# Optimization experiments

Measured on AMD Instinct MI355X. Metric: run time of the kernel, lower is better.

The kernel has to match this reference:

```python
import jax, jax.numpy as jnp
import numpy as np

COS_EPS = 1e-08


def setup_inputs() -> dict:
    key = jax.random.key(0)
    k1, k2, k3, k4, k5 = jax.random.split(key, 5)
    B, N, C = 4, 4096, 128
    q_node = jax.random.normal(k1, (B, N, C), dtype=jnp.float32)
    k_node = jax.random.normal(k2, (B, N, C), dtype=jnp.float32)
    v_node = jax.random.normal(k3, (B, N, C), dtype=jnp.float32)
    # shared Linear(h_dim, h_dim): torch default init scale ~ 1/sqrt(C)
    W = jax.random.normal(k4, (C, C), dtype=jnp.float32) / jnp.sqrt(jnp.float32(C))
    b = jax.random.normal(k5, (C,), dtype=jnp.float32) / jnp.sqrt(jnp.float32(C))
    return {"q_node": q_node, "k_node": k_node, "v_node": v_node, "W": W, "b": b}


def reference(q_node, k_node, v_node, W, b):
    # shared projection applied to q, k, v
    q = jnp.einsum('bnc,cd->bnd', q_node, W.T) + b
    k = jnp.einsum('bnc,cd->bnd', k_node, W.T) + b
    v = jnp.einsum('bnc,cd->bnd', v_node, W.T) + b
    # cosine similarity scores: [B, Nq, Nk]
    qn = jnp.linalg.norm(q, axis=2, keepdims=True)        # [B, Nq, 1]
    kn = jnp.linalg.norm(k, axis=2, keepdims=True)        # [B, Nk, 1]
    scores = jnp.einsum('bqc,bkc->bqk', q, k)
    cos_sim = scores / (qn * jnp.swapaxes(kn, 1, 2) + COS_EPS)
    # sum-normalization (not softmax)
    edge_weight = cos_sim / (cos_sim.sum(axis=2, keepdims=True) + 1e-08)
    # weighted aggregation: [B, Nq, C]
    return jnp.einsum('bqk,bkc->bqc', edge_weight, v)
```

## Files before the change

kernel.cpp:

```cpp
#include <hip/hip_runtime.h>

#define BB 4
#define NN 4096
#define CC 128
#define NROWS (BB * NN)

#define QN_OFF  0
#define QP_OFF  (QN_OFF + NROWS)
#define MM_OFF  (QP_OFF + NROWS * CC)
#define KS_OFF  (MM_OFF + BB * CC * CC)
#define PP_OFF  (KS_OFF + BB * CC)
#define KP_OFF  (PP_OFF + 256 * CC * CC)

typedef __attribute__((ext_vector_type(8))) short short8;
typedef __attribute__((ext_vector_type(4))) float f32x4;

__device__ __forceinline__ float dot4(const float4 x, const float4 k)
{
    return x.x * k.x + x.y * k.y + x.z * k.z + x.w * k.w;
}

__device__ __forceinline__ unsigned short f2bf(float f)
{
    union { float f; unsigned u; } v; v.f = f;
    unsigned r = (v.u + 0x7fffu + ((v.u >> 16) & 1u)) >> 16;
    return (unsigned short)r;
}
__device__ __forceinline__ float bf2f(unsigned short h)
{
    union { unsigned u; float f; } v; v.u = ((unsigned)h) << 16;
    return v.f;
}

__global__ __launch_bounds__(512, 1) void projpb_kernel(
    const float* __restrict__ q_node, const float* __restrict__ k_node,
    const float* __restrict__ v_node, const float* __restrict__ W,
    const float* __restrict__ bias, float* __restrict__ ws)
{
    __shared__ __align__(16) unsigned short Wsp[3 * CC * CC];
    __shared__ float4 red[512];
    unsigned short* Whi = Wsp;
    unsigned short* Wmd = Wsp + CC * CC;
    unsigned short* Wlo = Wsp + 2 * CC * CC;

    const int tid = threadIdx.x;

    for (int e = tid; e < CC * CC; e += 512) {
        int col = e >> 7, k = e & 127;
        float wv = W[e];
        unsigned short hi = f2bf(wv);
        float r1 = wv - bf2f(hi);
        unsigned short md = f2bf(r1);
        unsigned short lo = f2bf(r1 - bf2f(md));
        int idx = (col << 7) + ((((k >> 3) ^ (col & 7)) << 3) | (k & 7));
        Whi[idx] = hi; Wmd[idx] = md; Wlo[idx] = lo;
    }

    const int blk  = blockIdx.x;
    const int base = blk * 64;
    const int w    = tid >> 6;
    const int lane = tid & 63;
    const int l15  = lane & 15;
    const int lg   = lane >> 4;
    const bool isq = (w < 4);
    const int rt   = w & 3;
    const float* X = isq ? q_node : k_node;
    const int arow = base + rt * 16 + l15;

    f32x4 acc[8];
#pragma unroll
    for (int ct = 0; ct < 8; ct++) {
        float b = bias[ct * 16 + l15];
        acc[ct] = (f32x4){b, b, b, b};
    }

    __syncthreads();

    const float* Xr = X + (size_t)arow * CC;
#pragma unroll
    for (int ks = 0; ks < 4; ks++) {
        const int k0 = ks * 32 + lg * 8;
        float4 xa = *(const float4*)(Xr + k0);
        float4 xb = *(const float4*)(Xr + k0 + 4);
        float xs[8] = {xa.x, xa.y, xa.z, xa.w, xb.x, xb.y, xb.z, xb.w};
        short8 Ahi, Amd, Alo;
#pragma unroll
        for (int j = 0; j < 8; j++) {
            unsigned short h = f2bf(xs[j]);
            float r1 = xs[j] - bf2f(h);
            unsigned short m = f2bf(r1);
            Ahi[j] = (short)h;
            Amd[j] = (short)m;
            Alo[j] = (short)f2bf(r1 - bf2f(m));
        }
        const int slot = ks * 4 + lg;
#pragma unroll
        for (int ct = 0; ct < 8; ct++) {
            int col  = ct * 16 + l15;
            int fidx = (col << 7) + ((slot ^ (col & 7)) << 3);
            short8 Bhi = *(const short8*)(Whi + fidx);
            short8 Bmd = *(const short8*)(Wmd + fidx);
            short8 Blo = *(const short8*)(Wlo + fidx);
            acc[ct] = __builtin_amdgcn_mfma_f32_16x16x32_bf16(Ahi, Bhi, acc[ct], 0, 0, 0);
            acc[ct] = __builtin_amdgcn_mfma_f32_16x16x32_bf16(Ahi, Bmd, acc[ct], 0, 0, 0);
            acc[ct] = __builtin_amdgcn_mfma_f32_16x16x32_bf16(Amd, Bhi, acc[ct], 0, 0, 0);
            acc[ct] = __builtin_amdgcn_mfma_f32_16x16x32_bf16(Ahi, Blo, acc[ct], 0, 0, 0);
            acc[ct] = __builtin_amdgcn_mfma_f32_16x16x32_bf16(Amd, Bmd, acc[ct], 0, 0, 0);
            acc[ct] = __builtin_amdgcn_mfma_f32_16x16x32_bf16(Alo, Bhi, acc[ct], 0, 0, 0);
        }
    }

    float ss[4];
#pragma unroll
    for (int r = 0; r < 4; r++) {
        float t = 0.f;
#pragma unroll
        for (int ct = 0; ct < 8; ct++) t += acc[ct][r] * acc[ct][r];
#pragma unroll
        for (int off = 8; off > 0; off >>= 1) t += __shfl_xor(t, off, 16);
        ss[r] = t;
    }

    if (isq) {
#pragma unroll
        for (int r = 0; r < 4; r++) {
            int gr = base + rt * 16 + lg * 4 + r;
            float* qp = ws + QP_OFF + (size_t)gr * CC;
#pragma unroll
            for (int ct = 0; ct < 8; ct++) qp[ct * 16 + l15] = acc[ct][r];
            if (l15 == 0) ws[QN_OFF + gr] = sqrtf(ss[r]);
        }
    }

    __syncthreads();

    float* Khs = (float*)Wsp;
    float* Vs  = Khs + 8192;

    if (!isq) {
#pragma unroll
        for (int r = 0; r < 4; r++) {
            float inv = 1.0f / sqrtf(ss[r]);
            int lr = rt * 16 + lg * 4 + r;
            float* kp = Khs + lr * CC;
#pragma unroll
            for (int ct = 0; ct < 8; ct++) kp[ct * 16 + l15] = acc[ct][r] * inv;
        }
    }

    const int c4v = tid & 31, nrv = tid >> 5;
    const float* Vp = v_node + (size_t)base * CC;
#pragma unroll
    for (int i = 0; i < 4; i++) {
        int n = nrv + i * 16;
        ((float4*)(Vs + n * CC))[c4v] = ((const float4*)(Vp + (size_t)n * CC))[c4v];
    }
    __syncthreads();

    float4 ksum4 = make_float4(0.f, 0.f, 0.f, 0.f);
#pragma unroll
    for (int i = 0; i < 4; i++) {
        int n = nrv + i * 16;
        float4 kv = ((const float4*)(Khs + n * CC))[c4v];
        ksum4.x += kv.x; ksum4.y += kv.y; ksum4.z += kv.z; ksum4.w += kv.w;
    }

    const int dg2 = tid & 15, cg = tid >> 4;
    float a2[4][8];
#pragma unroll
    for (int i = 0; i < 4; i++)
#pragma unroll
        for (int j = 0; j < 8; j++) a2[i][j] = 0.f;

#define P2L(ka, va, vb, n)                                  \
    ka = *(const float4*)(Khs + (n) * CC + 4 * cg);         \
    va = *(const float4*)(Vs + (n) * CC + 4 * dg2);         \
    vb = *(const float4*)(Vs + (n) * CC + 64 + 4 * dg2);
#define P2F(ka, va, vb)                                     \
    {  float kc[4] = {ka.x, ka.y, ka.z, ka.w};              \
       float vd[8] = {va.x, va.y, va.z, va.w,               \
                      vb.x, vb.y, vb.z, vb.w};              \
       _Pragma("unroll")                                    \
       for (int i = 0; i < 4; i++)                          \
           { _Pragma("unroll")                              \
             for (int j = 0; j < 8; j++)                    \
                 a2[i][j] += kc[i] * vd[j]; } }

    {
        float4 kaA, vaA, vbA, kaB, vaB, vbB;
        P2L(kaA, vaA, vbA, 0)
        for (int n = 0; n <= 60; n += 2) {
            P2L(kaB, vaB, vbB, n + 1)
            P2F(kaA, vaA, vbA)
            P2L(kaA, vaA, vbA, n + 2)
            P2F(kaB, vaB, vbB)
        }
        P2L(kaB, vaB, vbB, 63)
        P2F(kaA, vaA, vbA)
        P2F(kaB, vaB, vbB)
    }
#undef P2L
#undef P2F

    float* pp = ws + PP_OFF + (size_t)blk * (CC * CC);
#pragma unroll
    for (int i = 0; i < 4; i++) {
        int c = 4 * cg + i;
        *(float4*)(pp + c * CC + 4 * dg2) =
            make_float4(a2[i][0], a2[i][1], a2[i][2], a2[i][3]);
        *(float4*)(pp + c * CC + 64 + 4 * dg2) =
            make_float4(a2[i][4], a2[i][5], a2[i][6], a2[i][7]);
    }

    red[nrv * 32 + c4v] = ksum4;
    __syncthreads();
    if (tid < 32) {
        float4 sm = red[tid];
#pragma unroll
        for (int i = 1; i < 16; i++) {
            float4 t = red[i * 32 + tid];
            sm.x += t.x; sm.y += t.y; sm.z += t.z; sm.w += t.w;
        }
        ((float4*)(ws + KP_OFF + (size_t)blk * CC))[tid] = sm;
    }
}

__global__ __launch_bounds__(256) void mchain_kernel(const float* __restrict__ W,
                                                     const float* __restrict__ bias,
                                                     float* __restrict__ ws)
{
    __shared__ float4 W4s[CC * 32];
    __shared__ float4 m0q[4][2][32];
    __shared__ float m0row[2][CC];
    __shared__ float kpart[4];
    __shared__ float ksl[2];
    const int tid = threadIdx.x;
    const int b = blockIdx.y, x = blockIdx.x;
    const int c0 = x * 2;

    for (int idx = tid; idx < CC * 32; idx += 256) {
        int e = idx >> 5, d4 = idx & 31;
        W4s[(e << 5) + (d4 ^ (e & 31))] = ((const float4*)W)[idx];
    }

    {
        const int q  = tid >> 6;
        const int r  = (tid >> 5) & 1;
        const int c4 = tid & 31;
        const float4* pp = (const float4*)(ws + PP_OFF
                         + (size_t)(b * 64 + q * 16) * (CC * CC)
                         + (size_t)(c0 + r) * CC) + c4;
        float4 s0 = make_float4(0.f, 0.f, 0.f, 0.f);
#pragma unroll 4
        for (int p = 0; p < 16; p++) {
            float4 t = pp[(size_t)p * (CC * CC / 4)];
            s0.x += t.x; s0.y += t.y; s0.z += t.z; s0.w += t.w;
        }
        m0q[q][r][c4] = s0;
    }

    {
        const int rr = tid >> 7, p = tid & 127;
        float v = 0.f;
        if (p < 64) v = ws[KP_OFF + (size_t)(b * 64 + p) * CC + c0 + rr];
#pragma unroll
        for (int off = 32; off > 0; off >>= 1) v += __shfl_xor(v, off, 64);
        if ((tid & 63) == 0) kpart[tid >> 6] = v;
    }
    __syncthreads();

    if (tid < 64) {
        const int r = tid >> 5, c4 = tid & 31;
        float4 a = m0q[0][r][c4], bq = m0q[1][r][c4];
        float4 c = m0q[2][r][c4], d = m0q[3][r][c4];
        float4 s;
        s.x = (a.x + bq.x) + (c.x + d.x);
        s.y = (a.y + bq.y) + (c.y + d.y);
        s.z = (a.z + bq.z) + (c.z + d.z);
        s.w = (a.w + bq.w) + (c.w + d.w);
        ((float4*)&m0row[r][0])[c4] = s;
    }
    if (tid < 2) {
        float s = kpart[tid * 2] + kpart[tid * 2 + 1];
        ksl[tid] = s;
        ws[KS_OFF + b * CC + c0 + tid] = s;
    }
    __syncthreads();

    const int r = tid >> 7, e = tid & 127;
    const float4* mr = (const float4*)m0row[r];
    float m = 0.f;
#pragma unroll
    for (int d4 = 0; d4 < 32; d4++) {
        float4 a4 = mr[d4];
        float4 w4 = W4s[(e << 5) + (d4 ^ (e & 31))];
        m += a4.x * w4.x + a4.y * w4.y + a4.z * w4.z + a4.w * w4.w;
    }
    m += ksl[r] * bias[e];
    ws[MM_OFF + (size_t)b * CC * CC + (size_t)(c0 + r) * CC + e] = m;
}

__global__ __launch_bounds__(512, 1) void out_kernel(const float* __restrict__ ws,
                                                     float* __restrict__ out)
{
    __shared__ __align__(16) unsigned short Msp[3 * CC * CC];
    __shared__ float Ksl[CC];
    unsigned short* Mhi = Msp;
    unsigned short* Mmd = Msp + CC * CC;
    unsigned short* Mlo = Msp + 2 * CC * CC;

    const int tid = threadIdx.x;
    const int blk = blockIdx.x;
    const int b  = blk >> 6;
    const int r0 = (blk & 63) * 64;
    const float* M = ws + MM_OFF + (size_t)b * CC * CC;

    for (int e = tid; e < CC * CC; e += 512) {
        int k = e >> 7, col = e & 127;
        float mv = M[e];
        unsigned short hi = f2bf(mv);
        float r1 = mv - bf2f(hi);
        unsigned short md = f2bf(r1);
        unsigned short lo = f2bf(r1 - bf2f(md));
        int idx = (col << 7) + ((((k >> 3) ^ (col & 7)) << 3) | (k & 7));
        Mhi[idx] = hi; Mmd[idx] = md; Mlo[idx] = lo;
    }
    if (tid < CC) Ksl[tid] = ws[KS_OFF + b * CC + tid];

    const int w    = tid >> 6;
    const int lane = tid & 63;
    const int l15  = lane & 15;
    const int lg   = lane >> 4;
    const int rt   = w & 3;
    const int ch   = w >> 2;

    const int arow = r0 + rt * 16 + l15;
    const float* Xr = ws + QP_OFF + ((size_t)b * NN + arow) * CC;

    f32x4 acc[4];
#pragma unroll
    for (int ct = 0; ct < 4; ct++) acc[ct] = (f32x4){0.f, 0.f, 0.f, 0.f};
    float sp = 0.f;

    __syncthreads();

#pragma unroll
    for (int ks = 0; ks < 4; ks++) {
        const int k0 = ks * 32 + lg * 8;
        float4 xa = *(const float4*)(Xr + k0);
        float4 xb = *(const float4*)(Xr + k0 + 4);
        float xs[8] = {xa.x, xa.y, xa.z, xa.w, xb.x, xb.y, xb.z, xb.w};
        short8 Ahi, Amd, Alo;
#pragma unroll
        for (int j = 0; j < 8; j++) {
            unsigned short h = f2bf(xs[j]);
            float r1 = xs[j] - bf2f(h);
            unsigned short m = f2bf(r1);
            Ahi[j] = (short)h;
            Amd[j] = (short)m;
            Alo[j] = (short)f2bf(r1 - bf2f(m));
            sp += xs[j] * Ksl[k0 + j];
        }
        const int slot = ks * 4 + lg;
#pragma unroll
        for (int ct = 0; ct < 4; ct++) {
            int col  = ch * 64 + ct * 16 + l15;
            int fidx = (col << 7) + ((slot ^ (col & 7)) << 3);
            short8 Bhi = *(const short8*)(Mhi + fidx);
            short8 Bmd = *(const short8*)(Mmd + fidx);
            short8 Blo = *(const short8*)(Mlo + fidx);
            acc[ct] = __builtin_amdgcn_mfma_f32_16x16x32_bf16(Ahi, Bhi, acc[ct], 0, 0, 0);
            acc[ct] = __builtin_amdgcn_mfma_f32_16x16x32_bf16(Ahi, Bmd, acc[ct], 0, 0, 0);
            acc[ct] = __builtin_amdgcn_mfma_f32_16x16x32_bf16(Amd, Bhi, acc[ct], 0, 0, 0);
            acc[ct] = __builtin_amdgcn_mfma_f32_16x16x32_bf16(Ahi, Blo, acc[ct], 0, 0, 0);
            acc[ct] = __builtin_amdgcn_mfma_f32_16x16x32_bf16(Amd, Bmd, acc[ct], 0, 0, 0);
            acc[ct] = __builtin_amdgcn_mfma_f32_16x16x32_bf16(Alo, Bhi, acc[ct], 0, 0, 0);
        }
    }

    sp += __shfl_xor(sp, 16, 64);
    sp += __shfl_xor(sp, 32, 64);

#pragma unroll
    for (int r = 0; r < 4; r++) {
        const int rowt = lg * 4 + r;
        float srow = __shfl(sp, rowt, 64);
        const int gr = r0 + rt * 16 + rowt;
        float qn = ws[QN_OFF + (size_t)b * NN + gr];
        float inv = 1.0f / (srow + 1e-8f * qn);
        float* op = out + ((size_t)b * NN + gr) * CC + ch * 64;
#pragma unroll
        for (int ct = 0; ct < 4; ct++)
            op[ct * 16 + l15] = acc[ct][r] * inv;
    }
}

extern "C" void kernel_launch(void* const* d_in, const int* in_sizes, int n_in,
                              void* d_out, int out_size, void* d_ws, size_t ws_size,
                              hipStream_t stream)
{
    const float* q_node = (const float*)d_in[0];
    const float* k_node = (const float*)d_in[1];
    const float* v_node = (const float*)d_in[2];
    const float* W      = (const float*)d_in[3];
    const float* bias   = (const float*)d_in[4];
    float* out = (float*)d_out;
    float* ws  = (float*)d_ws;

    projpb_kernel<<<256, 512, 0, stream>>>(q_node, k_node, v_node, W, bias, ws);
    mchain_kernel<<<dim3(64, BB), 256, 0, stream>>>(W, bias, ws);
    out_kernel<<<256, 512, 0, stream>>>(ws, out);
}
```

Measured before the change: 122.0 us.

## Compute per-block K^T V partial with split-bf16 MFMA instead of FP32 FMA

The per-block outer-product accumulation of normalized K and V (128x128 over 64 rows) moves from a scalar FP32 FMA loop to bf16 MFMA instructions. Each operand is split into three bf16 parts so that six MFMAs per tile approximate FP32 accuracy. K and V are written into swizzled shared-memory layouts, and the per-block K column sums are now reduced with wave shuffles. The split conversion adds ALU work and smaller LDS stores, and it risks small accuracy loss compared with exact FP32.

```diff
diff --git a/kernel.cpp b/kernel.cpp
--- a/kernel.cpp
+++ b/kernel.cpp
@@ -15,11 +15,6 @@
 typedef __attribute__((ext_vector_type(8))) short short8;
 typedef __attribute__((ext_vector_type(4))) float f32x4;
 
-__device__ __forceinline__ float dot4(const float4 x, const float4 k)
-{
-    return x.x * k.x + x.y * k.y + x.z * k.z + x.w * k.w;
-}
-
 __device__ __forceinline__ unsigned short f2bf(float f)
 {
     union { float f; unsigned u; } v; v.f = f;
@@ -38,7 +33,7 @@
     const float* __restrict__ bias, float* __restrict__ ws)
 {
     __shared__ __align__(16) unsigned short Wsp[3 * CC * CC];
-    __shared__ float4 red[512];
+    __shared__ float redf[512];
     unsigned short* Whi = Wsp;
     unsigned short* Wmd = Wsp + CC * CC;
     unsigned short* Wlo = Wsp + 2 * CC * CC;
@@ -134,94 +129,104 @@
 
     __syncthreads();
 
-    float* Khs = (float*)Wsp;
-    float* Vs  = Khs + 8192;
+    unsigned short* Ahi_p = Wsp;
+    unsigned short* Amd_p = Wsp + 8192;
+    unsigned short* Alo_p = Wsp + 16384;
+    unsigned short* Bhi_p = Wsp + 24576;
+    unsigned short* Bmd_p = Wsp + 32768;
+    unsigned short* Blo_p = Wsp + 40960;
 
     if (!isq) {
+        float ksp[8] = {0.f, 0.f, 0.f, 0.f, 0.f, 0.f, 0.f, 0.f};
 #pragma unroll
         for (int r = 0; r < 4; r++) {
             float inv = 1.0f / sqrtf(ss[r]);
-            int lr = rt * 16 + lg * 4 + r;
-            float* kp = Khs + lr * CC;
-#pragma unroll
-            for (int ct = 0; ct < 8; ct++) kp[ct * 16 + l15] = acc[ct][r] * inv;
-        }
-    }
-
-    const int c4v = tid & 31, nrv = tid >> 5;
-    const float* Vp = v_node + (size_t)base * CC;
-#pragma unroll
-    for (int i = 0; i < 4; i++) {
-        int n = nrv + i * 16;
-        ((float4*)(Vs + n * CC))[c4v] = ((const float4*)(Vp + (size_t)n * CC))[c4v];
-    }
-    __syncthreads();
-
-    float4 ksum4 = make_float4(0.f, 0.f, 0.f, 0.f);
-#pragma unroll
-    for (int i = 0; i < 4; i++) {
-        int n = nrv + i * 16;
-        float4 kv = ((const float4*)(Khs + n * CC))[c4v];
-        ksum4.x += kv.x; ksum4.y += kv.y; ksum4.z += kv.z; ksum4.w += kv.w;
-    }
-
-    const int dg2 = tid & 15, cg = tid >> 4;
-    float a2[4][8];
-#pragma unroll
-    for (int i = 0; i < 4; i++)
-#pragma unroll
-        for (int j = 0; j < 8; j++) a2[i][j] = 0.f;
-
-#define P2L(ka, va, vb, n)                                  \
-    ka = *(const float4*)(Khs + (n) * CC + 4 * cg);         \
-    va = *(const float4*)(Vs + (n) * CC + 4 * dg2);         \
-    vb = *(const float4*)(Vs + (n) * CC + 64 + 4 * dg2);
-#define P2F(ka, va, vb)                                     \
-    {  float kc[4] = {ka.x, ka.y, ka.z, ka.w};              \
-       float vd[8] = {va.x, va.y, va.z, va.w,               \
-                      vb.x, vb.y, vb.z, vb.w};              \
-       _Pragma("unroll")                                    \
-       for (int i = 0; i < 4; i++)                          \
-           { _Pragma("unroll")                              \
-             for (int j = 0; j < 8; j++)                    \
-                 a2[i][j] += kc[i] * vd[j]; } }
+            int n = rt * 16 + lg * 4 + r;
+#pragma unroll
+            for (int ct = 0; ct < 8; ct++) {
+                int c = ct * 16 + l15;
+                float val = acc[ct][r] * inv;
+                unsigned short h = f2bf(val);
+                float r1 = val - bf2f(h);
+                unsigned short m = f2bf(r1);
+                unsigned short l = f2bf(r1 - bf2f(m));
+                int idx = (c << 6) + ((((n >> 3) ^ (c & 7)) << 3) | (n & 7));
+                Ahi_p[idx] = h; Amd_p[idx] = m; Alo_p[idx] = l;
+                ksp[ct] += val;
+            }
+        }
+#pragma unroll
+        for (int ct = 0; ct < 8; ct++) {
+            ksp[ct] += __shfl_xor(ksp[ct], 16, 64);
+            ksp[ct] += __shfl_xor(ksp[ct], 32, 64);
+            if (lg == 0) redf[(rt * 8 + ct) * 16 + l15] = ksp[ct];
+        }
+    }
 
     {
-        float4 kaA, vaA, vbA, kaB, vaB, vbB;
-        P2L(kaA, vaA, vbA, 0)
-        for (int n = 0; n <= 60; n += 2) {
-            P2L(kaB, vaB, vbB, n + 1)
-            P2F(kaA, vaA, vbA)
-            P2L(kaA, vaA, vbA, n + 2)
-            P2F(kaB, vaB, vbB)
-        }
-        P2L(kaB, vaB, vbB, 63)
-        P2F(kaA, vaA, vbA)
-        P2F(kaB, vaB, vbB)
-    }
-#undef P2L
-#undef P2F
-
-    float* pp = ws + PP_OFF + (size_t)blk * (CC * CC);
-#pragma unroll
-    for (int i = 0; i < 4; i++) {
-        int c = 4 * cg + i;
-        *(float4*)(pp + c * CC + 4 * dg2) =
-            make_float4(a2[i][0], a2[i][1], a2[i][2], a2[i][3]);
-        *(float4*)(pp + c * CC + 64 + 4 * dg2) =
-            make_float4(a2[i][4], a2[i][5], a2[i][6], a2[i][7]);
-    }
-
-    red[nrv * 32 + c4v] = ksum4;
-    __syncthreads();
-    if (tid < 32) {
-        float4 sm = red[tid];
-#pragma unroll
-        for (int i = 1; i < 16; i++) {
-            float4 t = red[i * 32 + tid];
-            sm.x += t.x; sm.y += t.y; sm.z += t.z; sm.w += t.w;
-        }
-        ((float4*)(ws + KP_OFF + (size_t)blk * CC))[tid] = sm;
+        const int c4v = tid & 31, nrv = (tid >> 5) & 15;
+        const float* Vp = v_node + (size_t)base * CC;
+#pragma unroll
+        for (int i = 0; i < 4; i++) {
+            int n = nrv + i * 16;
+#pragma unroll
+            for (int j = 0; j < 4; j++) {
+                int d = c4v + 32 * j;
+                float val = Vp[(size_t)n * CC + d];
+                unsigned short h = f2bf(val);
+                float r1 = val - bf2f(h);
+                unsigned short m = f2bf(r1);
+                unsigned short l = f2bf(r1 - bf2f(m));
+                int idx = (d << 6) + ((((n >> 3) ^ (d & 7)) << 3) | (n & 7));
+                Bhi_p[idx] = h; Bmd_p[idx] = m; Blo_p[idx] = l;
+            }
+        }
+    }
+    __syncthreads();
+
+    {
+        f32x4 macc[8];
+#pragma unroll
+        for (int dt = 0; dt < 8; dt++) macc[dt] = (f32x4){0.f, 0.f, 0.f, 0.f};
+        const int crow = w * 16 + l15;
+#pragma unroll
+        for (int ks2 = 0; ks2 < 2; ks2++) {
+            const int slot = ks2 * 4 + lg;
+            int aidx = (crow << 6) + ((slot ^ (crow & 7)) << 3);
+            short8 Ah = *(const short8*)(Ahi_p + aidx);
+            short8 Am = *(const short8*)(Amd_p + aidx);
+            short8 Al = *(const short8*)(Alo_p + aidx);
+#pragma unroll
+            for (int dt = 0; dt < 8; dt++) {
+                int d = dt * 16 + l15;
+                int bidx = (d << 6) + ((slot ^ (d & 7)) << 3);
+                short8 Bh = *(const short8*)(Bhi_p + bidx);
+                short8 Bm = *(const short8*)(Bmd_p + bidx);
+                short8 Bl = *(const short8*)(Blo_p + bidx);
+                macc[dt] = __builtin_amdgcn_mfma_f32_16x16x32_bf16(Ah, Bh, macc[dt], 0, 0, 0);
+                macc[dt] = __builtin_amdgcn_mfma_f32_16x16x32_bf16(Ah, Bm, macc[dt], 0, 0, 0);
+                macc[dt] = __builtin_amdgcn_mfma_f32_16x16x32_bf16(Am, Bh, macc[dt], 0, 0, 0);
+                macc[dt] = __builtin_amdgcn_mfma_f32_16x16x32_bf16(Ah, Bl, macc[dt], 0, 0, 0);
+                macc[dt] = __builtin_amdgcn_mfma_f32_16x16x32_bf16(Am, Bm, macc[dt], 0, 0, 0);
+                macc[dt] = __builtin_amdgcn_mfma_f32_16x16x32_bf16(Al, Bh, macc[dt], 0, 0, 0);
+            }
+        }
+
+        float* pp = ws + PP_OFF + (size_t)blk * (CC * CC);
+#pragma unroll
+        for (int dt = 0; dt < 8; dt++)
+#pragma unroll
+            for (int r = 0; r < 4; r++)
+                pp[(size_t)(w * 16 + lg * 4 + r) * CC + dt * 16 + l15] = macc[dt][r];
+    }
+
+    if (w == 0 && lg == 0) {
+#pragma unroll
+        for (int ct = 0; ct < 8; ct++) {
+            float s = redf[(0 * 8 + ct) * 16 + l15] + redf[(1 * 8 + ct) * 16 + l15]
+                    + redf[(2 * 8 + ct) * 16 + l15] + redf[(3 * 8 + ct) * 16 + l15];
+            ws[KP_OFF + (size_t)blk * CC + ct * 16 + l15] = s;
+        }
     }
 }
 
```

Result: no change. 121.6 us (-0.3%).
